# Optimization experiments

Hardware: AMD Instinct MI355X
Metric: run time of the kernel (lower is better)

## Reference

```python
import jax, jax.numpy as jnp
import numpy as np

N = 10000          # num_stations / nodes
E = 320000         # edges
IN_DIM = 32
HID = 64
SEQ = 168
OUT_DIM = 10000


def _gcn_conv(x, W, b, src, dst, num_nodes):
    """PyG GCNConv: add self-loops, sym-normalize, gather-scatter aggregate."""
    loop = jnp.arange(num_nodes)
    s = jnp.concatenate([src, loop])
    d = jnp.concatenate([dst, loop])
    deg = jax.ops.segment_sum(jnp.ones_like(d, dtype=x.dtype), d, num_segments=num_nodes)
    dinv = jnp.where(deg > 0, jax.lax.rsqrt(deg), 0.0)
    norm = dinv[s] * dinv[d]                      # [E+N]
    h = x @ W.T                                   # [N, out] linear (no bias inside)
    msg = h[s] * norm[:, None]                    # gather + scale
    out = jax.ops.segment_sum(msg, d, num_segments=num_nodes)  # scatter-add
    return out + b


def setup_inputs() -> dict:
    key = jax.random.key(0)
    ks = jax.random.split(key, 16)
    sc = 0.05
    return {
        "x": jax.random.normal(ks[0], (N, IN_DIM), jnp.float32),
        "edge_index": jax.random.randint(ks[1], (2, E), 0, N, jnp.int64),
        "rain_history": jax.random.normal(ks[2], (1, SEQ), jnp.float32),
        "future_rain": jax.random.normal(ks[3], (1, 1), jnp.float32),
        "W1": jax.random.normal(ks[4], (HID, IN_DIM), jnp.float32) * sc,
        "b1": jnp.zeros((HID,), jnp.float32),
        "W2": jax.random.normal(ks[5], (HID, HID), jnp.float32) * sc,
        "b2": jnp.zeros((HID,), jnp.float32),
        "wf1_W": jax.random.normal(ks[6], (HID, SEQ + 1), jnp.float32) * sc,
        "wf1_b": jnp.zeros((HID,), jnp.float32),
        "wf2_W": jax.random.normal(ks[7], (HID, HID), jnp.float32) * sc,
        "wf2_b": jnp.zeros((HID,), jnp.float32),
        "of1_W": jax.random.normal(ks[8], (HID * 2, HID * N + HID), jnp.float32) * 0.001,
        "of1_b": jnp.zeros((HID * 2,), jnp.float32),
        "of2_W": jax.random.normal(ks[9], (OUT_DIM, HID * 2), jnp.float32) * sc,
        "of2_b": jnp.zeros((OUT_DIM,), jnp.float32),
    }


def reference(x, edge_index, rain_history, future_rain,
              W1, b1, W2, b2, wf1_W, wf1_b, wf2_W, wf2_b,
              of1_W, of1_b, of2_W, of2_b):
    src, dst = edge_index[0], edge_index[1]
    num_nodes = x.shape[0]
    h = jax.nn.relu(_gcn_conv(x, W1, b1, src, dst, num_nodes))
    h = jax.nn.relu(_gcn_conv(h, W2, b2, src, dst, num_nodes))
    h = jnp.clip(h, -10.0, 10.0)
    node_features = h.reshape(1, -1)                        # [1, N*HID]
    weather_input = jnp.concatenate([rain_history, future_rain], axis=1)  # [1, SEQ+1]
    w = jax.nn.relu(weather_input @ wf1_W.T + wf1_b)
    weather_features = w @ wf2_W.T + wf2_b                  # [1, HID]
    combined = jnp.concatenate([node_features, weather_features], axis=1)
    o = jax.nn.relu(combined @ of1_W.T + of1_b)
    out = o @ of2_W.T + of2_b                               # [1, OUT_DIM]
    return out.squeeze(0)
```

## Files before the change

### kernel.cpp

```cpp
#include <hip/hip_runtime.h>

#define N_NODES 10000
#define N_EDGES 320000
#define HID 64
#define IN_DIM 32
#define SEQ 168
#define OUT_DIM 10000
#define OF1_COLS 640064
#define NODE_COLS 640000
#define BUCKET 128
#define FILLB  1250
#define LIN1B  2500
#define NSLOT  64

typedef __attribute__((ext_vector_type(4))) float f32x4;

__global__ __launch_bounds__(256) void k_fill_lin1_weather(
        const int* __restrict__ eidx, int* __restrict__ cursor, int* __restrict__ csr,
        const float* __restrict__ x, const float* __restrict__ W1, float* __restrict__ hlin,
        const float* __restrict__ rain, const float* __restrict__ fut,
        const float* __restrict__ w1W, const float* __restrict__ w1b,
        const float* __restrict__ w2W, const float* __restrict__ w2b,
        const float* __restrict__ of1W, float* __restrict__ wtail) {
    int t = threadIdx.x;
    int b = blockIdx.x;
    if (b < FILLB) {
        int e = b * 256 + t;
        if (e < N_EDGES) {
            int s = eidx[e];
            int d = eidx[N_EDGES + e];
            int slot = atomicAdd(&cursor[d], 1);
            csr[d * BUCKET + slot] = s;
        }
    } else if (b < FILLB + LIN1B) {
        __shared__ float Wl[64][33];
        __shared__ float xs[4][32];
        for (int i = t; i < 64 * 32; i += 256) Wl[i >> 5][i & 31] = W1[i];
        int node0 = (b - FILLB) * 4;
        if (t < 128) {
            int n = t >> 5, k = t & 31;
            xs[n][k] = x[(node0 + n) * IN_DIM + k];
        }
        __syncthreads();
        int nl = t >> 6, j = t & 63;
        float acc = 0.f;
#pragma unroll
        for (int k = 0; k < 32; k++) acc += xs[nl][k] * Wl[j][k];
        hlin[(node0 + nl) * HID + j] = acc;
    } else {
        __shared__ float wi[SEQ + 1];
        __shared__ float w1[64];
        __shared__ float wf[64];
        if (t < SEQ) wi[t] = rain[t];
        if (t == SEQ) wi[SEQ] = fut[0];
        __syncthreads();
        if (t < 64) {
            float acc = w1b[t];
            for (int i = 0; i < SEQ + 1; i++) acc += w1W[t * (SEQ + 1) + i] * wi[i];
            w1[t] = fmaxf(acc, 0.f);
        }
        __syncthreads();
        if (t < 64) {
            float acc2 = w2b[t];
#pragma unroll
            for (int i = 0; i < 64; i++) acc2 += w2W[t * 64 + i] * w1[i];
            wf[t] = acc2;
        }
        __syncthreads();
        if (t < 128) {
            const float* Wt = of1W + (size_t)t * OF1_COLS + NODE_COLS;
            float s = 0.f;
#pragma unroll
            for (int w = 0; w < 64; w++) s += Wt[w] * wf[w];
            wtail[t] = s;
        }
    }
}

__global__ __launch_bounds__(256) void k_agg1_lin2(
        const float* __restrict__ hlin, const int* __restrict__ cnt,
        const int* __restrict__ csr, const float* __restrict__ b1,
        const float* __restrict__ W2, float* __restrict__ h2) {
    __shared__ float Wl[64][65];
    __shared__ float xs[4][64];
    int t = threadIdx.x;
    for (int i = t; i < 64 * 64; i += 256) Wl[i >> 6][i & 63] = W2[i];
    int wid = t >> 6, lane = t & 63;
    int n = blockIdx.x * 4 + wid;
    int deg = cnt[n];
    float dn = rsqrtf((float)(deg + 1));
    float acc = hlin[n * HID + lane] * dn;
    const int* row = csr + n * BUCKET;
    for (int base = 0; base < deg; base += 64) {
        int idx = base + lane;
        int sv = row[(idx < deg) ? idx : 0];
        float dv = (idx < deg) ? rsqrtf((float)(cnt[sv] + 1)) : 0.f;
        int m = deg - base;
        if (m > 64) m = 64;
        int m4 = (m + 3) & ~3;
        for (int j = 0; j < m4; j += 4) {
            int s0 = __shfl(sv, j, 64), s1 = __shfl(sv, j + 1, 64);
            int s2 = __shfl(sv, j + 2, 64), s3 = __shfl(sv, j + 3, 64);
            float d0 = __shfl(dv, j, 64), d1 = __shfl(dv, j + 1, 64);
            float d2 = __shfl(dv, j + 2, 64), d3 = __shfl(dv, j + 3, 64);
            float v0 = hlin[s0 * HID + lane];
            float v1 = hlin[s1 * HID + lane];
            float v2 = hlin[s2 * HID + lane];
            float v3 = hlin[s3 * HID + lane];
            acc = fmaf(d0, v0, acc);
            acc = fmaf(d1, v1, acc);
            acc = fmaf(d2, v2, acc);
            acc = fmaf(d3, v3, acc);
        }
    }
    float v = fmaxf(dn * acc + b1[lane], 0.f);
    xs[wid][lane] = v;
    __syncthreads();
    float a2 = 0.f;
#pragma unroll
    for (int k = 0; k < 64; k++) a2 += xs[wid][k] * Wl[lane][k];
    h2[n * HID + lane] = a2;
}

__global__ __launch_bounds__(256) void k_agg2_of1(
        const float* __restrict__ h2, const int* __restrict__ cnt,
        const int* __restrict__ csr, const float* __restrict__ b2,
        const float* __restrict__ of1W, float* __restrict__ o_pre) {
    __shared__ float xs[4][64];
    int t = threadIdx.x;
    int wid = t >> 6, lane = t & 63;
    int n = blockIdx.x * 4 + wid;
    int deg = cnt[n];
    float dn = rsqrtf((float)(deg + 1));
    float acc = h2[n * HID + lane] * dn;
    const int* row = csr + n * BUCKET;
    for (int base = 0; base < deg; base += 64) {
        int idx = base + lane;
        int sv = row[(idx < deg) ? idx : 0];
        float dv = (idx < deg) ? rsqrtf((float)(cnt[sv] + 1)) : 0.f;
        int m = deg - base;
        if (m > 64) m = 64;
        int m4 = (m + 3) & ~3;
        for (int j = 0; j < m4; j += 4) {
            int s0 = __shfl(sv, j, 64), s1 = __shfl(sv, j + 1, 64);
            int s2 = __shfl(sv, j + 2, 64), s3 = __shfl(sv, j + 3, 64);
            float d0 = __shfl(dv, j, 64), d1 = __shfl(dv, j + 1, 64);
            float d2 = __shfl(dv, j + 2, 64), d3 = __shfl(dv, j + 3, 64);
            float v0 = h2[s0 * HID + lane];
            float v1 = h2[s1 * HID + lane];
            float v2 = h2[s2 * HID + lane];
            float v3 = h2[s3 * HID + lane];
            acc = fmaf(d0, v0, acc);
            acc = fmaf(d1, v1, acc);
            acc = fmaf(d2, v2, acc);
            acc = fmaf(d3, v3, acc);
        }
    }
    float v = dn * acc + b2[lane];
    v = fmaxf(v, 0.f);
    v = fminf(v, 10.f);
    xs[wid][lane] = v;
    __syncthreads();

    f32x4 c = ((const f32x4*)xs)[lane];
    size_t colbase = (size_t)blockIdx.x * 256;
    float* oslot = o_pre + (size_t)(blockIdx.x & (NSLOT - 1)) * 128;
    int j0w = wid * 32;
#pragma unroll 2
    for (int g = 0; g < 8; g++) {
        int j0 = j0w + g * 4;
        const f32x4* W0 = (const f32x4*)(of1W + (size_t)(j0 + 0) * OF1_COLS + colbase);
        const f32x4* W1r = (const f32x4*)(of1W + (size_t)(j0 + 1) * OF1_COLS + colbase);
        const f32x4* W2r = (const f32x4*)(of1W + (size_t)(j0 + 2) * OF1_COLS + colbase);
        const f32x4* W3r = (const f32x4*)(of1W + (size_t)(j0 + 3) * OF1_COLS + colbase);
        f32x4 w0 = __builtin_nontemporal_load(&W0[lane]);
        f32x4 w1 = __builtin_nontemporal_load(&W1r[lane]);
        f32x4 w2 = __builtin_nontemporal_load(&W2r[lane]);
        f32x4 w3 = __builtin_nontemporal_load(&W3r[lane]);
        float a0 = w0.x * c.x + w0.y * c.y + w0.z * c.z + w0.w * c.w;
        float a1 = w1.x * c.x + w1.y * c.y + w1.z * c.z + w1.w * c.w;
        float a2 = w2.x * c.x + w2.y * c.y + w2.z * c.z + w2.w * c.w;
        float a3 = w3.x * c.x + w3.y * c.y + w3.z * c.z + w3.w * c.w;
        float a0s = a0 + __shfl_xor(a0, 32, 64);
        float a1s = a1 + __shfl_xor(a1, 32, 64);
        float a2s = a2 + __shfl_xor(a2, 32, 64);
        float a3s = a3 + __shfl_xor(a3, 32, 64);
        float c01 = (lane < 32) ? a0s : a1s;
        float c23 = (lane < 32) ? a2s : a3s;
        float c01b = c01 + __shfl_xor(c01, 16, 64);
        float c23b = c23 + __shfl_xor(c23, 16, 64);
        float e = ((lane & 16) == 0) ? c01b : c23b;
        e += __shfl_xor(e, 8, 64);
        e += __shfl_xor(e, 4, 64);
        e += __shfl_xor(e, 2, 64);
        e += __shfl_xor(e, 1, 64);
        if ((lane & 15) == 0) {
            int roff = ((lane & 16) ? 2 : 0) + ((lane & 32) ? 1 : 0);
            atomicAdd(&oslot[j0 + roff], e);
        }
    }
}

__global__ __launch_bounds__(256) void k_of2(const float* __restrict__ W, const float* __restrict__ of2b,
                                             const float* __restrict__ o_pre, const float* __restrict__ of1b,
                                             const float* __restrict__ wtail, float* __restrict__ out) {
    __shared__ float os[128];
    int t = threadIdx.x;
    if (t < 128) {
        float s = of1b[t] + wtail[t];
#pragma unroll
        for (int cidx = 0; cidx < NSLOT; cidx++) s += o_pre[cidx * 128 + t];
        os[t] = fmaxf(s, 0.f);
    }
    __syncthreads();
    int k = blockIdx.x * 256 + t;
    if (k >= OUT_DIM) return;
    const f32x4* Wr = (const f32x4*)(W + (size_t)k * 128);
    float acc = of2b[k];
#pragma unroll
    for (int i = 0; i < 32; i++) {
        f32x4 wv = __builtin_nontemporal_load(&Wr[i]);
        int base = i * 4;
        acc += wv.x * os[base + 0] + wv.y * os[base + 1] + wv.z * os[base + 2] + wv.w * os[base + 3];
    }
    out[k] = acc;
}

extern "C" void kernel_launch(void* const* d_in, const int* in_sizes, int n_in,
                              void* d_out, int out_size, void* d_ws, size_t ws_size,
                              hipStream_t stream) {
    const float* x    = (const float*)d_in[0];
    const int*  eidx  = (const int*)d_in[1];
    const float* rain = (const float*)d_in[2];
    const float* fut  = (const float*)d_in[3];
    const float* W1   = (const float*)d_in[4];
    const float* b1   = (const float*)d_in[5];
    const float* W2   = (const float*)d_in[6];
    const float* b2   = (const float*)d_in[7];
    const float* wf1W = (const float*)d_in[8];
    const float* wf1b = (const float*)d_in[9];
    const float* wf2W = (const float*)d_in[10];
    const float* wf2b = (const float*)d_in[11];
    const float* of1W = (const float*)d_in[12];
    const float* of1b = (const float*)d_in[13];
    const float* of2W = (const float*)d_in[14];
    const float* of2b = (const float*)d_in[15];
    float* out = (float*)d_out;

    char* p = (char*)d_ws;
    int*   cursor = (int*)(p + 0);
    float* o_pre  = (float*)(p + 40000);
    int*   csr    = (int*)(p + 73728);
    float* hlin   = (float*)(p + 5242880);
    float* h2     = (float*)(p + 7864320);
    float* wtail  = (float*)(p + 10485760);

    hipMemsetAsync(p, 0, 72768, stream);

    k_fill_lin1_weather<<<FILLB + LIN1B + 1, 256, 0, stream>>>(
        eidx, cursor, csr, x, W1, hlin, rain, fut, wf1W, wf1b, wf2W, wf2b, of1W, wtail);

    k_agg1_lin2<<<N_NODES / 4, 256, 0, stream>>>(hlin, cursor, csr, b1, W2, h2);
    k_agg2_of1<<<N_NODES / 4, 256, 0, stream>>>(h2, cursor, csr, b2, of1W, o_pre);

    k_of2<<<(OUT_DIM + 255) / 256, 256, 0, stream>>>(of2W, of2b, o_pre, of1b, wtail, out);
}
```

Measured before the change: 510.5 us.

## Prefetch of1 weights before aggregation and pre-scale h2 by source norm

Issues the first group of of1 weight loads before the layer-2 neighbour aggregation and double-buffers the remaining weight groups, so the large streaming read of the weight matrix overlaps the gather and the reductions. It also folds the source-side degree normalisation into h2 when h2 is written, which removes the per-edge rsqrt, the cnt[] gather and the shuffles from the aggregation loop. The cost is higher register pressure from the two weight buffers, which could lower occupancy.

```diff
diff --git a/kernel.cpp b/kernel.cpp
--- a/kernel.cpp
+++ b/kernel.cpp
@@ -119,7 +119,7 @@
     float a2 = 0.f;
 #pragma unroll
     for (int k = 0; k < 64; k++) a2 += xs[wid][k] * Wl[lane][k];
-    h2[n * HID + lane] = a2;
+    h2[n * HID + lane] = a2 * dn;
 }
 
 __global__ __launch_bounds__(256) void k_agg2_of1(
@@ -129,31 +129,43 @@
     __shared__ float xs[4][64];
     int t = threadIdx.x;
     int wid = t >> 6, lane = t & 63;
+    size_t colbase = (size_t)blockIdx.x * 256;
+    int j0w = wid * 32;
+
+#define LOADG(buf, g) do {                                                                  \
+        int j0_ = j0w + (g) * 4;                                                            \
+        buf[0] = __builtin_nontemporal_load((const f32x4*)(of1W + (size_t)(j0_ + 0) * OF1_COLS + colbase) + lane); \
+        buf[1] = __builtin_nontemporal_load((const f32x4*)(of1W + (size_t)(j0_ + 1) * OF1_COLS + colbase) + lane); \
+        buf[2] = __builtin_nontemporal_load((const f32x4*)(of1W + (size_t)(j0_ + 2) * OF1_COLS + colbase) + lane); \
+        buf[3] = __builtin_nontemporal_load((const f32x4*)(of1W + (size_t)(j0_ + 3) * OF1_COLS + colbase) + lane); \
+    } while (0)
+
+    f32x4 bufA[4], bufB[4];
+    LOADG(bufA, 0);
+
     int n = blockIdx.x * 4 + wid;
     int deg = cnt[n];
     float dn = rsqrtf((float)(deg + 1));
-    float acc = h2[n * HID + lane] * dn;
+    float acc = h2[n * HID + lane];
     const int* row = csr + n * BUCKET;
     for (int base = 0; base < deg; base += 64) {
         int idx = base + lane;
         int sv = row[(idx < deg) ? idx : 0];
-        float dv = (idx < deg) ? rsqrtf((float)(cnt[sv] + 1)) : 0.f;
         int m = deg - base;
         if (m > 64) m = 64;
-        int m4 = (m + 3) & ~3;
-        for (int j = 0; j < m4; j += 4) {
+        int mfull = m & ~3;
+        for (int j = 0; j < mfull; j += 4) {
             int s0 = __shfl(sv, j, 64), s1 = __shfl(sv, j + 1, 64);
             int s2 = __shfl(sv, j + 2, 64), s3 = __shfl(sv, j + 3, 64);
-            float d0 = __shfl(dv, j, 64), d1 = __shfl(dv, j + 1, 64);
-            float d2 = __shfl(dv, j + 2, 64), d3 = __shfl(dv, j + 3, 64);
             float v0 = h2[s0 * HID + lane];
             float v1 = h2[s1 * HID + lane];
             float v2 = h2[s2 * HID + lane];
             float v3 = h2[s3 * HID + lane];
-            acc = fmaf(d0, v0, acc);
-            acc = fmaf(d1, v1, acc);
-            acc = fmaf(d2, v2, acc);
-            acc = fmaf(d3, v3, acc);
+            acc += v0; acc += v1; acc += v2; acc += v3;
+        }
+        for (int j = mfull; j < m; j++) {
+            int s = __shfl(sv, j, 64);
+            acc += h2[s * HID + lane];
         }
     }
     float v = dn * acc + b2[lane];
@@ -163,42 +175,43 @@
     __syncthreads();
 
     f32x4 c = ((const f32x4*)xs)[lane];
-    size_t colbase = (size_t)blockIdx.x * 256;
     float* oslot = o_pre + (size_t)(blockIdx.x & (NSLOT - 1)) * 128;
-    int j0w = wid * 32;
-#pragma unroll 2
-    for (int g = 0; g < 8; g++) {
-        int j0 = j0w + g * 4;
-        const f32x4* W0 = (const f32x4*)(of1W + (size_t)(j0 + 0) * OF1_COLS + colbase);
-        const f32x4* W1r = (const f32x4*)(of1W + (size_t)(j0 + 1) * OF1_COLS + colbase);
-        const f32x4* W2r = (const f32x4*)(of1W + (size_t)(j0 + 2) * OF1_COLS + colbase);
-        const f32x4* W3r = (const f32x4*)(of1W + (size_t)(j0 + 3) * OF1_COLS + colbase);
-        f32x4 w0 = __builtin_nontemporal_load(&W0[lane]);
-        f32x4 w1 = __builtin_nontemporal_load(&W1r[lane]);
-        f32x4 w2 = __builtin_nontemporal_load(&W2r[lane]);
-        f32x4 w3 = __builtin_nontemporal_load(&W3r[lane]);
-        float a0 = w0.x * c.x + w0.y * c.y + w0.z * c.z + w0.w * c.w;
-        float a1 = w1.x * c.x + w1.y * c.y + w1.z * c.z + w1.w * c.w;
-        float a2 = w2.x * c.x + w2.y * c.y + w2.z * c.z + w2.w * c.w;
-        float a3 = w3.x * c.x + w3.y * c.y + w3.z * c.z + w3.w * c.w;
-        float a0s = a0 + __shfl_xor(a0, 32, 64);
-        float a1s = a1 + __shfl_xor(a1, 32, 64);
-        float a2s = a2 + __shfl_xor(a2, 32, 64);
-        float a3s = a3 + __shfl_xor(a3, 32, 64);
-        float c01 = (lane < 32) ? a0s : a1s;
-        float c23 = (lane < 32) ? a2s : a3s;
-        float c01b = c01 + __shfl_xor(c01, 16, 64);
-        float c23b = c23 + __shfl_xor(c23, 16, 64);
-        float e = ((lane & 16) == 0) ? c01b : c23b;
-        e += __shfl_xor(e, 8, 64);
-        e += __shfl_xor(e, 4, 64);
-        e += __shfl_xor(e, 2, 64);
-        e += __shfl_xor(e, 1, 64);
-        if ((lane & 15) == 0) {
-            int roff = ((lane & 16) ? 2 : 0) + ((lane & 32) ? 1 : 0);
-            atomicAdd(&oslot[j0 + roff], e);
-        }
-    }
+
+#define COMPG(buf, g) do {                                                                  \
+        int j0_ = j0w + (g) * 4;                                                            \
+        float a0 = buf[0].x * c.x + buf[0].y * c.y + buf[0].z * c.z + buf[0].w * c.w;       \
+        float a1 = buf[1].x * c.x + buf[1].y * c.y + buf[1].z * c.z + buf[1].w * c.w;       \
+        float a2 = buf[2].x * c.x + buf[2].y * c.y + buf[2].z * c.z + buf[2].w * c.w;       \
+        float a3 = buf[3].x * c.x + buf[3].y * c.y + buf[3].z * c.z + buf[3].w * c.w;       \
+        float a0s = a0 + __shfl_xor(a0, 32, 64);                                            \
+        float a1s = a1 + __shfl_xor(a1, 32, 64);                                            \
+        float a2s = a2 + __shfl_xor(a2, 32, 64);                                            \
+        float a3s = a3 + __shfl_xor(a3, 32, 64);                                            \
+        float c01 = (lane < 32) ? a0s : a1s;                                                \
+        float c23 = (lane < 32) ? a2s : a3s;                                                \
+        float c01b = c01 + __shfl_xor(c01, 16, 64);                                         \
+        float c23b = c23 + __shfl_xor(c23, 16, 64);                                         \
+        float e = ((lane & 16) == 0) ? c01b : c23b;                                         \
+        e += __shfl_xor(e, 8, 64);                                                          \
+        e += __shfl_xor(e, 4, 64);                                                          \
+        e += __shfl_xor(e, 2, 64);                                                          \
+        e += __shfl_xor(e, 1, 64);                                                          \
+        if ((lane & 15) == 0) {                                                             \
+            int roff = ((lane & 16) ? 2 : 0) + ((lane & 32) ? 1 : 0);                       \
+            atomicAdd(&oslot[j0_ + roff], e);                                               \
+        }                                                                                   \
+    } while (0)
+
+    LOADG(bufB, 1); COMPG(bufA, 0);
+    LOADG(bufA, 2); COMPG(bufB, 1);
+    LOADG(bufB, 3); COMPG(bufA, 2);
+    LOADG(bufA, 4); COMPG(bufB, 3);
+    LOADG(bufB, 5); COMPG(bufA, 4);
+    LOADG(bufA, 6); COMPG(bufB, 5);
+    LOADG(bufB, 7); COMPG(bufA, 6);
+    COMPG(bufB, 7);
+#undef LOADG
+#undef COMPG
 }
 
 __global__ __launch_bounds__(256) void k_of2(const float* __restrict__ W, const float* __restrict__ of2b,
```

New measurement: 509.3 us. About the same (-0.2%).
